# Performance work log

Hardware: AMD Instinct MI355X
Metric: run time of the kernel (lower is better)

Reference implementation:

```python
import jax, jax.numpy as jnp
import numpy as np

L, P, D, NH, RBF, NL = 256, 1024, 256, 4, 50, 2
HD = D // NH
EPS = 1e-5


def _layernorm(x, g, b):
    mu = x.mean(-1, keepdims=True)
    var = ((x - mu) ** 2).mean(-1, keepdims=True)
    return (x - mu) * jax.lax.rsqrt(var + EPS) * g + b


def setup_inputs() -> dict:
    key = jax.random.key(0)
    ks = iter(jax.random.split(key, 64))
    def nrm(shape, s=0.02):
        return jax.random.normal(next(ks), shape, dtype=jnp.float32) * s
    inp = {
        "protein_features": jax.random.normal(next(ks), (1, P, 20), jnp.float32),
        "ligand_features": jax.random.normal(next(ks), (1, L, 20), jnp.float32),
        "protein_positions": jax.random.normal(next(ks), (1, P, 3), jnp.float32),
        "ligand_positions": jax.random.normal(next(ks), (1, L, 3), jnp.float32),
        "pair_rbf": jax.random.uniform(next(ks), (1, L, P, RBF), jnp.float32),
        # encoders
        "pe_w1": nrm((20, D)), "pe_b1": jnp.zeros((D,)),
        "pe_w2": nrm((D, D)), "pe_b2": jnp.zeros((D,)),
        "le_w1": nrm((20, D)), "le_b1": jnp.zeros((D,)),
        "le_w2": nrm((D, D)), "le_b2": jnp.zeros((D,)),
        # cross-attn layers stacked over NL
        "qw": nrm((NL, D, D)), "qb": jnp.zeros((NL, D)),
        "kw": nrm((NL, D, D)), "kb": jnp.zeros((NL, D)),
        "vw": nrm((NL, D, D)), "vb": jnp.zeros((NL, D)),
        "rw": nrm((NL, RBF, NH)), "rb": jnp.zeros((NL, NH)),
        "ow": nrm((NL, D, D)), "ob": jnp.zeros((NL, D)),
        "ln_g": jnp.ones((NL, D)), "ln_b": jnp.zeros((NL, D)),
        # gated pooling
        "pg_w1": nrm((D, D // 2)), "pg_b1": jnp.zeros((D // 2,)),
        "pg_w2": nrm((D // 2, 1)), "pg_b2": jnp.zeros((1,)),
        # heads
        "af_w1": nrm((D, D)), "af_b1": jnp.zeros((D,)),
        "af_w2": nrm((D, 1)), "af_b2": jnp.zeros((1,)),
        "cf_w1": nrm((D, D // 2)), "cf_b1": jnp.zeros((D // 2,)),
        "cf_w2": nrm((D // 2, 1)), "cf_b2": jnp.zeros((1,)),
        "iw1": nrm((2 * D + RBF, D)), "ib1": jnp.zeros((D,)),
        "iw2": nrm((D, 5)), "ib2": jnp.zeros((5,)),
    }
    return inp


def reference(protein_features, ligand_features, protein_positions, ligand_positions,
              pair_rbf, pe_w1, pe_b1, pe_w2, pe_b2, le_w1, le_b1, le_w2, le_b2,
              qw, qb, kw, kb, vw, vb, rw, rb, ow, ob, ln_g, ln_b,
              pg_w1, pg_b1, pg_w2, pg_b2, af_w1, af_b1, af_w2, af_b2,
              cf_w1, cf_b1, cf_w2, cf_b2, iw1, ib1, iw2, ib2):
    pf = protein_features[0]          # [P, 20]
    lf = ligand_features[0]           # [L, 20]
    rbf = pair_rbf[0]                 # [L, P, RBF]

    prot_h = jax.nn.silu(pf @ pe_w1 + pe_b1) @ pe_w2 + pe_b2   # [P, D]
    lig_h = jax.nn.silu(lf @ le_w1 + le_b1) @ le_w2 + le_b2    # [L, D]

    scale = float(HD) ** 0.5
    attn_w = None
    for i in range(NL):
        Q = (lig_h @ qw[i] + qb[i]).reshape(L, NH, HD)
        K = (prot_h @ kw[i] + kb[i]).reshape(P, NH, HD)
        V = (prot_h @ vw[i] + vb[i]).reshape(P, NH, HD)
        scores = jnp.einsum('lhd,phd->lph', Q, K) / scale      # [L, P, NH]
        scores = scores + (rbf @ rw[i] + rb[i])                # RBF additive bias per head
        attn_w = jax.nn.softmax(scores, axis=1)                # softmax over protein axis
        attended = jnp.einsum('lph,phd->lhd', attn_w, V).reshape(L, D)
        lig_h = _layernorm(lig_h + attended @ ow[i] + ob[i], ln_g[i], ln_b[i])

    gate_logits = jnp.tanh(lig_h @ pg_w1 + pg_b1) @ pg_w2 + pg_b2  # [L, 1]
    gate = jax.nn.softmax(gate_logits, axis=0)
    complex_repr = (gate * lig_h).sum(axis=0, keepdims=True)        # [1, D]

    pkd = jax.nn.silu(complex_repr @ af_w1 + af_b1) @ af_w2 + af_b2
    conf = jax.nn.sigmoid(jax.nn.silu(complex_repr @ cf_w1 + cf_b1) @ cf_w2 + cf_b2)
    docking_score = pkd * conf

    lig_exp = jnp.broadcast_to(lig_h[:, None, :], (L, P, D))
    prot_exp = jnp.broadcast_to(prot_h[None, :, :], (L, P, D))
    pair_input = jnp.concatenate([lig_exp, prot_exp, rbf], axis=-1)  # [L, P, 2D+RBF]
    imap = jax.nn.sigmoid(jax.nn.silu(pair_input @ iw1 + ib1) @ iw2 + ib2)

    attn_out = attn_w.mean(axis=-1).reshape(1, L * P)
    return (docking_score, pkd, conf, imap[None], attn_out)
```

## Files before the change

### kernel.cpp

```cpp
#include <hip/hip_runtime.h>
#include <math.h>

#define LN_ 256
#define PN_ 1024
#define DN_ 256
#define NH_ 4
#define RBF_N 50
#define NL_ 2
#define HD_ 64
#define EPSV 1e-5f
#define LP_ (LN_ * PN_)

__device__ __forceinline__ float fast_sigmoid(float x){ return 1.f/(1.f+__expf(-x)); }
__device__ __forceinline__ float fast_silu(float x){ return x/(1.f+__expf(-x)); }

struct GSeg {
  const float* A; const float* W; const float* bias; float* C;
  int K; int act; int transOut;
};
struct GArgs { GSeg s[3]; int b0, b1; };

__global__ __launch_bounds__(256) void gemm8(GArgs ga)
{
  extern __shared__ float sA[];
  int bid = blockIdx.x;
  int si = (bid < ga.b0) ? 0 : (bid < ga.b1 ? 1 : 2);
  int base = (si == 0) ? 0 : ((si == 1) ? ga.b0 : ga.b1);
  GSeg sg = ga.s[si];
  int row0 = (bid - base) * 8;
  int K = sg.K;
  int t = threadIdx.x;
  for (int idx = t; idx < 8 * K; idx += 256) {
    int r = idx / K, k = idx - r * K;
    sA[idx] = sg.A[(size_t)(row0 + r) * K + k];
  }
  __syncthreads();
  float acc[8];
  float bv = sg.bias ? sg.bias[t] : 0.f;
  #pragma unroll
  for (int r = 0; r < 8; r++) acc[r] = bv;
  for (int k = 0; k < K; k++) {
    float w = sg.W[(size_t)k * DN_ + t];
    #pragma unroll
    for (int r = 0; r < 8; r++) acc[r] = fmaf(sA[r * K + k], w, acc[r]);
  }
  #pragma unroll
  for (int r = 0; r < 8; r++) {
    float v = acc[r];
    if (sg.act == 1) v = fast_silu(v);
    if (sg.transOut) sg.C[(size_t)t * PN_ + row0 + r] = v;
    else             sg.C[(size_t)(row0 + r) * DN_ + t] = v;
  }
}

__global__ __launch_bounds__(256) void rbf_transpose(
    const float* __restrict__ rbf, float* __restrict__ rbfT)
{
  __shared__ float ld[256][RBF_N + 1];
  int t = threadIdx.x;
  size_t base = (size_t)blockIdx.x << 8;
  const float* src = rbf + base * RBF_N;
  for (int i = 0; i < RBF_N; i++) {
    int fl = i * 256 + t;
    int row = fl / RBF_N, col = fl - row * RBF_N;
    ld[row][col] = src[fl];
  }
  __syncthreads();
  for (int k = 0; k < RBF_N; k++)
    rbfT[(size_t)k * LP_ + base + t] = ld[t][k];
}

__global__ __launch_bounds__(256) void scores_softmax_l(
    const float* __restrict__ Q, const float* __restrict__ Kt,
    const float* __restrict__ rbfT, const float* __restrict__ rw,
    const float* __restrict__ rb, float* __restrict__ attn,
    float* __restrict__ amean)
{
  int l = blockIdx.x, t = threadIdx.x, lane = t & 63, wv = t >> 6;
  __shared__ float qs[DN_];
  __shared__ float rws[NH_][RBF_N];
  __shared__ float redm[16], reds[16];
  qs[t] = Q[(size_t)l * DN_ + t];
  if (t < RBF_N * NH_) rws[t & 3][t >> 2] = rw[t];
  __syncthreads();

  float sc[NH_][4];
  for (int i = 0; i < 4; i++) {
    int p = t + (i << 8);
    size_t idx = ((size_t)l << 10) + p;
    float s2[NH_] = {0.f, 0.f, 0.f, 0.f};
    #pragma unroll 10
    for (int k = 0; k < RBF_N; k++) {
      float rv = rbfT[(size_t)k * LP_ + idx];
      s2[0] = fmaf(rv, rws[0][k], s2[0]);
      s2[1] = fmaf(rv, rws[1][k], s2[1]);
      s2[2] = fmaf(rv, rws[2][k], s2[2]);
      s2[3] = fmaf(rv, rws[3][k], s2[3]);
    }
    #pragma unroll
    for (int h = 0; h < NH_; h++) {
      const float* kp = Kt + ((size_t)(h << 6) << 10) + p;
      float a = 0.f;
      #pragma unroll 8
      for (int d = 0; d < HD_; d++) a = fmaf(qs[(h << 6) + d], kp[(size_t)d << 10], a);
      sc[h][i] = a * 0.125f + s2[h] + rb[h];
    }
  }

  float mh[NH_];
  #pragma unroll
  for (int h = 0; h < NH_; h++) {
    float m = fmaxf(fmaxf(sc[h][0], sc[h][1]), fmaxf(sc[h][2], sc[h][3]));
    for (int o = 32; o > 0; o >>= 1) m = fmaxf(m, __shfl_xor(m, o));
    if (lane == 0) redm[h * 4 + wv] = m;
  }
  __syncthreads();
  #pragma unroll
  for (int h = 0; h < NH_; h++)
    mh[h] = fmaxf(fmaxf(redm[h * 4 + 0], redm[h * 4 + 1]),
                  fmaxf(redm[h * 4 + 2], redm[h * 4 + 3]));

  float e[NH_][4], inv[NH_];
  #pragma unroll
  for (int h = 0; h < NH_; h++) {
    float s = 0.f;
    #pragma unroll
    for (int i = 0; i < 4; i++) { e[h][i] = __expf(sc[h][i] - mh[h]); s += e[h][i]; }
    for (int o = 32; o > 0; o >>= 1) s += __shfl_xor(s, o);
    if (lane == 0) reds[h * 4 + wv] = s;
  }
  __syncthreads();
  #pragma unroll
  for (int h = 0; h < NH_; h++)
    inv[h] = 1.f / (reds[h * 4 + 0] + reds[h * 4 + 1] + reds[h * 4 + 2] + reds[h * 4 + 3]);

  #pragma unroll
  for (int h = 0; h < NH_; h++)
    for (int i = 0; i < 4; i++)
      attn[(((size_t)(l << 2) + h) << 10) + t + (i << 8)] = e[h][i] * inv[h];

  if (amean) {
    for (int i = 0; i < 4; i++) {
      float s = e[0][i] * inv[0] + e[1][i] * inv[1] + e[2][i] * inv[2] + e[3][i] * inv[3];
      amean[((size_t)l << 10) + t + (i << 8)] = s * 0.25f;
    }
  }
}

__global__ __launch_bounds__(256) void attend_proj_ln(
    const float* __restrict__ attn, const float* __restrict__ V,
    const float* __restrict__ ow, const float* __restrict__ ob,
    const float* __restrict__ g, const float* __restrict__ bb,
    float* __restrict__ lig)
{
  int l = blockIdx.x, t = threadIdx.x, lane = t & 63, wv = t >> 6;
  int h = t >> 6, d = t & 63;
  __shared__ float as[DN_];
  __shared__ float red[8];
  const float* aw = attn + (((size_t)(l << 2) + h) << 10);
  const float* Vp = V + (h << 6) + d;
  float acc = 0.f;
  #pragma unroll 8
  for (int p = 0; p < PN_; p++) acc = fmaf(aw[p], Vp[(size_t)p << 8], acc);
  as[t] = acc;
  __syncthreads();
  float acc2 = ob[t];
  #pragma unroll 4
  for (int k = 0; k < DN_; k++) acc2 = fmaf(as[k], ow[(size_t)(k << 8) + t], acc2);
  float x = lig[((size_t)l << 8) + t] + acc2;
  float sm = x;
  for (int o = 32; o > 0; o >>= 1) sm += __shfl_xor(sm, o);
  if (lane == 0) red[wv] = sm;
  __syncthreads();
  float mu = (red[0] + red[1] + red[2] + red[3]) * (1.f / DN_);
  float dx = x - mu;
  float v = dx * dx;
  for (int o = 32; o > 0; o >>= 1) v += __shfl_xor(v, o);
  if (lane == 0) red[4 + wv] = v;
  __syncthreads();
  float var = (red[4] + red[5] + red[6] + red[7]) * (1.f / DN_);
  lig[((size_t)l << 8) + t] = dx * (1.f / sqrtf(var + EPSV)) * g[t] + bb[t];
}

__global__ __launch_bounds__(128) void gate_logits_k(
    const float* __restrict__ lig, const float* __restrict__ w1,
    const float* __restrict__ b1, const float* __restrict__ w2,
    const float* __restrict__ b2, float* __restrict__ glog)
{
  int l = blockIdx.x, n = threadIdx.x, lane = n & 63, wv = n >> 6;
  __shared__ float ls[DN_];
  __shared__ float red[2];
  ls[n] = lig[(size_t)l * DN_ + n];
  ls[n + 128] = lig[(size_t)l * DN_ + n + 128];
  __syncthreads();
  float acc = b1[n];
  #pragma unroll 4
  for (int k = 0; k < DN_; k++) acc = fmaf(ls[k], w1[k * 128 + n], acc);
  float part = tanhf(acc) * w2[n];
  for (int o = 32; o > 0; o >>= 1) part += __shfl_xor(part, o);
  if (lane == 0) red[wv] = part;
  __syncthreads();
  if (n == 0) glog[l] = red[0] + red[1] + b2[0];
}

__global__ __launch_bounds__(256) void pool_heads(
    const float* __restrict__ lig, const float* __restrict__ glog,
    const float* __restrict__ afw1, const float* __restrict__ afb1,
    const float* __restrict__ afw2, const float* __restrict__ afb2,
    const float* __restrict__ cfw1, const float* __restrict__ cfb1,
    const float* __restrict__ cfw2, const float* __restrict__ cfb2,
    float* __restrict__ out)
{
  __shared__ float wsh[LN_];
  __shared__ float cr[DN_];
  __shared__ float h1s[DN_];
  __shared__ float h2s[128];
  __shared__ float red[8];
  int t = threadIdx.x, lane = t & 63, wv = t >> 6;
  float x = glog[t];
  float m = x;
  for (int o = 32; o > 0; o >>= 1) m = fmaxf(m, __shfl_xor(m, o));
  if (lane == 0) red[wv] = m;
  __syncthreads();
  m = fmaxf(fmaxf(red[0], red[1]), fmaxf(red[2], red[3]));
  float e = __expf(x - m);
  float s = e;
  for (int o = 32; o > 0; o >>= 1) s += __shfl_xor(s, o);
  if (lane == 0) red[4 + wv] = s;
  __syncthreads();
  s = red[4] + red[5] + red[6] + red[7];
  wsh[t] = e / s;
  __syncthreads();
  float acc = 0.f;
  #pragma unroll 4
  for (int l2 = 0; l2 < LN_; l2++) acc = fmaf(wsh[l2], lig[(size_t)l2 * DN_ + t], acc);
  cr[t] = acc;
  __syncthreads();
  float a = afb1[t];
  #pragma unroll 4
  for (int d = 0; d < DN_; d++) a = fmaf(cr[d], afw1[d * DN_ + t], a);
  h1s[t] = fast_silu(a);
  if (t < 128) {
    float c = cfb1[t];
    #pragma unroll 4
    for (int d = 0; d < DN_; d++) c = fmaf(cr[d], cfw1[d * 128 + t], c);
    h2s[t] = fast_silu(c);
  }
  __syncthreads();
  float pp = h1s[t] * afw2[t];
  for (int o = 32; o > 0; o >>= 1) pp += __shfl_xor(pp, o);
  if (lane == 0) red[wv] = pp;
  float cp = (t < 128) ? h2s[t] * cfw2[t] : 0.f;
  for (int o = 32; o > 0; o >>= 1) cp += __shfl_xor(cp, o);
  if (lane == 0) red[4 + wv] = cp;
  __syncthreads();
  if (t == 0) {
    float pkd = red[0] + red[1] + red[2] + red[3] + afb2[0];
    float cl  = red[4] + red[5] + red[6] + red[7] + cfb2[0];
    float conf = fast_sigmoid(cl);
    out[0] = pkd * conf;
    out[1] = pkd;
    out[2] = conf;
  }
}

__global__ __launch_bounds__(256, 4) void pair_main2(
    const float* __restrict__ A, const float* __restrict__ BT,
    const float* __restrict__ rbfT, const float* __restrict__ Wr,
    const float* __restrict__ w2, const float* __restrict__ ib2,
    float* __restrict__ imap)
{
  int t = threadIdx.x;
  int bid = blockIdx.x;
  int l = bid >> 2;
  int p = ((bid & 3) << 8) + t;
  size_t idx = ((size_t)l << 10) + p;
  const float* Ar = A + (l << 8);
  float acc[5];
  #pragma unroll
  for (int o = 0; o < 5; o++) acc[o] = ib2[o];

  for (int dt = 0; dt < 4; dt++) {
    int d0 = dt << 6;
    float h[64];
    #pragma unroll
    for (int j = 0; j < 64; j++)
      h[j] = Ar[d0 + j] + BT[(size_t)(d0 + j) * PN_ + p];

    #pragma unroll 2
    for (int k = 0; k < RBF_N; k++) {
      float rv = rbfT[(size_t)k * LP_ + idx];
      const float* wr = Wr + k * DN_ + d0;
      #pragma unroll
      for (int j = 0; j < 64; j++)
        h[j] = fmaf(rv, wr[j], h[j]);
    }

    #pragma unroll
    for (int j = 0; j < 64; j++) {
      float sh = fast_silu(h[j]);
      const float* w2r = w2 + (size_t)(d0 + j) * 5;
      #pragma unroll
      for (int o = 0; o < 5; o++) acc[o] = fmaf(sh, w2r[o], acc[o]);
    }
  }
  float* op = imap + idx * 5;
  #pragma unroll
  for (int o = 0; o < 5; o++) op[o] = fast_sigmoid(acc[o]);
}

extern "C" void kernel_launch(void* const* d_in, const int* in_sizes, int n_in,
                              void* d_out, int out_size, void* d_ws, size_t ws_size,
                              hipStream_t stream)
{
  const float* pf    = (const float*)d_in[0];
  const float* lf    = (const float*)d_in[1];
  const float* rbf   = (const float*)d_in[4];
  const float* pe_w1 = (const float*)d_in[5];
  const float* pe_b1 = (const float*)d_in[6];
  const float* pe_w2 = (const float*)d_in[7];
  const float* pe_b2 = (const float*)d_in[8];
  const float* le_w1 = (const float*)d_in[9];
  const float* le_b1 = (const float*)d_in[10];
  const float* le_w2 = (const float*)d_in[11];
  const float* le_b2 = (const float*)d_in[12];
  const float* qw = (const float*)d_in[13];
  const float* qb = (const float*)d_in[14];
  const float* kw = (const float*)d_in[15];
  const float* kb = (const float*)d_in[16];
  const float* vw = (const float*)d_in[17];
  const float* vb = (const float*)d_in[18];
  const float* rw = (const float*)d_in[19];
  const float* rb = (const float*)d_in[20];
  const float* ow = (const float*)d_in[21];
  const float* ob = (const float*)d_in[22];
  const float* ln_g = (const float*)d_in[23];
  const float* ln_b = (const float*)d_in[24];
  const float* pg_w1 = (const float*)d_in[25];
  const float* pg_b1 = (const float*)d_in[26];
  const float* pg_w2 = (const float*)d_in[27];
  const float* pg_b2 = (const float*)d_in[28];
  const float* af_w1 = (const float*)d_in[29];
  const float* af_b1 = (const float*)d_in[30];
  const float* af_w2 = (const float*)d_in[31];
  const float* af_b2 = (const float*)d_in[32];
  const float* cf_w1 = (const float*)d_in[33];
  const float* cf_b1 = (const float*)d_in[34];
  const float* cf_w2 = (const float*)d_in[35];
  const float* cf_b2 = (const float*)d_in[36];
  const float* iw1 = (const float*)d_in[37];
  const float* ib1 = (const float*)d_in[38];
  const float* iw2 = (const float*)d_in[39];
  const float* ib2 = (const float*)d_in[40];

  float* out = (float*)d_out;

  float* w = (float*)d_ws;
  size_t off = 0;
  float* prot_h = w + off; off += (size_t)PN_ * DN_;
  float* lig_h  = w + off; off += (size_t)LN_ * DN_;
  float* ph1    = w + off; off += (size_t)PN_ * DN_;
  float* lh1    = w + off; off += (size_t)LN_ * DN_;
  float* Qb     = w + off; off += (size_t)LN_ * DN_;
  float* Kt     = w + off; off += (size_t)DN_ * PN_;
  float* Vb     = w + off; off += (size_t)PN_ * DN_;
  float* attn   = w + off; off += (size_t)LN_ * NH_ * PN_;
  float* pairA  = w + off; off += (size_t)LN_ * DN_;
  float* glog   = w + off; off += LN_;
  off = (off + 255) & ~(size_t)255;
  float* rbfT   = w + off; off += (size_t)RBF_N * LP_;

  const int PB = PN_ / 8;
  const int LB = LN_ / 8;
  const size_t smax = 8 * DN_ * sizeof(float);

  rbf_transpose<<<LP_ / 256, 256, 0, stream>>>(rbf, rbfT);

  {
    GArgs ga;
    ga.s[0] = { pf, pe_w1, pe_b1, ph1, 20, 1, 0 };
    ga.s[1] = { lf, le_w1, le_b1, lh1, 20, 1, 0 };
    ga.s[2] = ga.s[1];
    ga.b0 = PB; ga.b1 = PB + LB;
    gemm8<<<PB + LB, 256, smax, stream>>>(ga);
  }
  {
    GArgs ga;
    ga.s[0] = { ph1, pe_w2, pe_b2, prot_h, DN_, 0, 0 };
    ga.s[1] = { lh1, le_w2, le_b2, lig_h, DN_, 0, 0 };
    ga.s[2] = ga.s[1];
    ga.b0 = PB; ga.b1 = PB + LB;
    gemm8<<<PB + LB, 256, smax, stream>>>(ga);
  }

  for (int i = 0; i < NL_; i++) {
    const size_t wo = (size_t)i * DN_ * DN_;
    {
      GArgs ga;
      ga.s[0] = { lig_h,  qw + wo, qb + i * DN_, Qb, DN_, 0, 0 };
      ga.s[1] = { prot_h, kw + wo, kb + i * DN_, Kt, DN_, 0, 1 };
      ga.s[2] = { prot_h, vw + wo, vb + i * DN_, Vb, DN_, 0, 0 };
      ga.b0 = LB; ga.b1 = LB + PB;
      gemm8<<<LB + 2 * PB, 256, smax, stream>>>(ga);
    }
    scores_softmax_l<<<LN_, 256, 0, stream>>>(
        Qb, Kt, rbfT, rw + (size_t)i * RBF_N * NH_, rb + i * NH_, attn,
        (i == NL_ - 1) ? (out + 3 + (size_t)LN_ * PN_ * 5) : nullptr);
    attend_proj_ln<<<LN_, 256, 0, stream>>>(attn, Vb, ow + wo, ob + i * DN_,
                                            ln_g + i * DN_, ln_b + i * DN_, lig_h);
  }

  gate_logits_k<<<LN_, 128, 0, stream>>>(lig_h, pg_w1, pg_b1, pg_w2, pg_b2, glog);
  pool_heads<<<1, 256, 0, stream>>>(lig_h, glog, af_w1, af_b1, af_w2, af_b2,
                                    cf_w1, cf_b1, cf_w2, cf_b2, out);

  {
    GArgs ga;
    ga.s[0] = { lig_h,  iw1,                       ib1,     pairA, DN_, 0, 0 };
    ga.s[1] = { prot_h, iw1 + (size_t)DN_ * DN_,   nullptr, Kt,    DN_, 0, 1 };
    ga.s[2] = ga.s[1];
    ga.b0 = LB; ga.b1 = LB + PB;
    gemm8<<<LB + PB, 256, smax, stream>>>(ga);
  }

  pair_main2<<<LP_ / 256, 256, 0, stream>>>(
      pairA, Kt, rbfT, iw1 + (size_t)2 * DN_ * DN_, iw2, ib2, out + 3);
}
```

Before: 732.7 us.

## Use bf16 MFMA for pair-map RBF projection and widen blocks in attention kernels

Replaces the scalar pair interaction kernel with one that stages RBF rows in LDS as bf16 and computes the RBF-to-hidden projection with 16x16x32 bf16 MFMA instructions, adding a one-off kernel that packs the RBF weight slice into transposed bf16. Separately, gemm8 now splits K across two thread halves, and the scores/softmax and attend/projection/layernorm kernels use 1024-thread blocks with one position per thread or split reductions. The goal is to remove the FMA-bound pair kernel and raise parallelism in the small per-ligand kernels. Running the RBF projection in bf16 lowers accuracy of the interaction map.

```diff
diff --git a/kernel.cpp b/kernel.cpp
--- a/kernel.cpp
+++ b/kernel.cpp
@@ -11,8 +11,16 @@
 #define EPSV 1e-5f
 #define LP_ (LN_ * PN_)
 
+typedef __attribute__((ext_vector_type(8))) short bf16x8;
+typedef __attribute__((ext_vector_type(4))) float f32x4;
+
 __device__ __forceinline__ float fast_sigmoid(float x){ return 1.f/(1.f+__expf(-x)); }
 __device__ __forceinline__ float fast_silu(float x){ return x/(1.f+__expf(-x)); }
+__device__ __forceinline__ short f2bf(float x){
+  union { float f; unsigned u; } v; v.f = x;
+  unsigned r = v.u + 0x7FFF + ((v.u >> 16) & 1);
+  return (short)(r >> 16);
+}
 
 struct GSeg {
   const float* A; const float* W; const float* bias; float* C;
@@ -20,9 +28,10 @@
 };
 struct GArgs { GSeg s[3]; int b0, b1; };
 
-__global__ __launch_bounds__(256) void gemm8(GArgs ga)
+__global__ __launch_bounds__(512) void gemm8(GArgs ga)
 {
   extern __shared__ float sA[];
+  __shared__ float part_[2][8][256];
   int bid = blockIdx.x;
   int si = (bid < ga.b0) ? 0 : (bid < ga.b1 ? 1 : 2);
   int base = (si == 0) ? 0 : ((si == 1) ? ga.b0 : ga.b1);
@@ -30,26 +39,33 @@
   int row0 = (bid - base) * 8;
   int K = sg.K;
   int t = threadIdx.x;
-  for (int idx = t; idx < 8 * K; idx += 256) {
+  int col = t & 255, half = t >> 8;
+  for (int idx = t; idx < 8 * K; idx += 512) {
     int r = idx / K, k = idx - r * K;
     sA[idx] = sg.A[(size_t)(row0 + r) * K + k];
   }
   __syncthreads();
   float acc[8];
-  float bv = sg.bias ? sg.bias[t] : 0.f;
-  #pragma unroll
-  for (int r = 0; r < 8; r++) acc[r] = bv;
-  for (int k = 0; k < K; k++) {
-    float w = sg.W[(size_t)k * DN_ + t];
+  #pragma unroll
+  for (int r = 0; r < 8; r++) acc[r] = 0.f;
+  int K2 = K >> 1;
+  for (int k = half * K2; k < half * K2 + K2; k++) {
+    float w = sg.W[(size_t)k * DN_ + col];
     #pragma unroll
     for (int r = 0; r < 8; r++) acc[r] = fmaf(sA[r * K + k], w, acc[r]);
   }
   #pragma unroll
-  for (int r = 0; r < 8; r++) {
-    float v = acc[r];
-    if (sg.act == 1) v = fast_silu(v);
-    if (sg.transOut) sg.C[(size_t)t * PN_ + row0 + r] = v;
-    else             sg.C[(size_t)(row0 + r) * DN_ + t] = v;
+  for (int r = 0; r < 8; r++) part_[half][r][col] = acc[r];
+  __syncthreads();
+  if (half == 0) {
+    float bv = sg.bias ? sg.bias[col] : 0.f;
+    #pragma unroll
+    for (int r = 0; r < 8; r++) {
+      float v = part_[0][r][col] + part_[1][r][col] + bv;
+      if (sg.act == 1) v = fast_silu(v);
+      if (sg.transOut) sg.C[(size_t)col * PN_ + row0 + r] = v;
+      else             sg.C[(size_t)(row0 + r) * DN_ + col] = v;
+    }
   }
 }
 
@@ -62,15 +78,23 @@
   const float* src = rbf + base * RBF_N;
   for (int i = 0; i < RBF_N; i++) {
     int fl = i * 256 + t;
-    int row = fl / RBF_N, col = fl - row * RBF_N;
-    ld[row][col] = src[fl];
+    int row = fl / RBF_N, colk = fl - row * RBF_N;
+    ld[row][colk] = src[fl];
   }
   __syncthreads();
   for (int k = 0; k < RBF_N; k++)
     rbfT[(size_t)k * LP_ + base + t] = ld[t][k];
 }
 
-__global__ __launch_bounds__(256) void scores_softmax_l(
+__global__ __launch_bounds__(256) void wr_pack(
+    const float* __restrict__ Wr, short* __restrict__ WT)
+{
+  int d = threadIdx.x;
+  for (int k = 0; k < 64; k++)
+    WT[d * 64 + k] = (k < RBF_N) ? f2bf(Wr[k * DN_ + d]) : (short)0;
+}
+
+__global__ __launch_bounds__(1024) void scores_softmax_l(
     const float* __restrict__ Q, const float* __restrict__ Kt,
     const float* __restrict__ rbfT, const float* __restrict__ rw,
     const float* __restrict__ rb, float* __restrict__ attn,
@@ -79,107 +103,109 @@
   int l = blockIdx.x, t = threadIdx.x, lane = t & 63, wv = t >> 6;
   __shared__ float qs[DN_];
   __shared__ float rws[NH_][RBF_N];
-  __shared__ float redm[16], reds[16];
-  qs[t] = Q[(size_t)l * DN_ + t];
+  __shared__ float redm[NH_][16], reds[NH_][16];
+  if (t < DN_) qs[t] = Q[(size_t)l * DN_ + t];
   if (t < RBF_N * NH_) rws[t & 3][t >> 2] = rw[t];
   __syncthreads();
 
-  float sc[NH_][4];
-  for (int i = 0; i < 4; i++) {
-    int p = t + (i << 8);
-    size_t idx = ((size_t)l << 10) + p;
-    float s2[NH_] = {0.f, 0.f, 0.f, 0.f};
-    #pragma unroll 10
-    for (int k = 0; k < RBF_N; k++) {
-      float rv = rbfT[(size_t)k * LP_ + idx];
-      s2[0] = fmaf(rv, rws[0][k], s2[0]);
-      s2[1] = fmaf(rv, rws[1][k], s2[1]);
-      s2[2] = fmaf(rv, rws[2][k], s2[2]);
-      s2[3] = fmaf(rv, rws[3][k], s2[3]);
-    }
-    #pragma unroll
-    for (int h = 0; h < NH_; h++) {
-      const float* kp = Kt + ((size_t)(h << 6) << 10) + p;
-      float a = 0.f;
-      #pragma unroll 8
-      for (int d = 0; d < HD_; d++) a = fmaf(qs[(h << 6) + d], kp[(size_t)d << 10], a);
-      sc[h][i] = a * 0.125f + s2[h] + rb[h];
-    }
-  }
-
+  int p = t;
+  size_t idx = ((size_t)l << 10) + p;
+  float s2[NH_] = {0.f, 0.f, 0.f, 0.f};
+  #pragma unroll 10
+  for (int k = 0; k < RBF_N; k++) {
+    float rv = rbfT[(size_t)k * LP_ + idx];
+    s2[0] = fmaf(rv, rws[0][k], s2[0]);
+    s2[1] = fmaf(rv, rws[1][k], s2[1]);
+    s2[2] = fmaf(rv, rws[2][k], s2[2]);
+    s2[3] = fmaf(rv, rws[3][k], s2[3]);
+  }
+  float sc[NH_];
+  #pragma unroll
+  for (int h = 0; h < NH_; h++) {
+    const float* kp = Kt + ((size_t)(h << 6) << 10) + p;
+    float a = 0.f;
+    #pragma unroll 8
+    for (int d = 0; d < HD_; d++) a = fmaf(qs[(h << 6) + d], kp[(size_t)d << 10], a);
+    sc[h] = a * 0.125f + s2[h] + rb[h];
+  }
+
+  #pragma unroll
+  for (int h = 0; h < NH_; h++) {
+    float m = sc[h];
+    for (int o = 32; o > 0; o >>= 1) m = fmaxf(m, __shfl_xor(m, o));
+    if (lane == 0) redm[h][wv] = m;
+  }
+  __syncthreads();
   float mh[NH_];
   #pragma unroll
   for (int h = 0; h < NH_; h++) {
-    float m = fmaxf(fmaxf(sc[h][0], sc[h][1]), fmaxf(sc[h][2], sc[h][3]));
-    for (int o = 32; o > 0; o >>= 1) m = fmaxf(m, __shfl_xor(m, o));
-    if (lane == 0) redm[h * 4 + wv] = m;
-  }
-  __syncthreads();
-  #pragma unroll
-  for (int h = 0; h < NH_; h++)
-    mh[h] = fmaxf(fmaxf(redm[h * 4 + 0], redm[h * 4 + 1]),
-                  fmaxf(redm[h * 4 + 2], redm[h * 4 + 3]));
-
-  float e[NH_][4], inv[NH_];
+    float m = redm[h][0];
+    for (int i = 1; i < 16; i++) m = fmaxf(m, redm[h][i]);
+    mh[h] = m;
+  }
+  float e[NH_];
   #pragma unroll
   for (int h = 0; h < NH_; h++) {
-    float s = 0.f;
-    #pragma unroll
-    for (int i = 0; i < 4; i++) { e[h][i] = __expf(sc[h][i] - mh[h]); s += e[h][i]; }
+    e[h] = __expf(sc[h] - mh[h]);
+    float s = e[h];
     for (int o = 32; o > 0; o >>= 1) s += __shfl_xor(s, o);
-    if (lane == 0) reds[h * 4 + wv] = s;
-  }
-  __syncthreads();
-  #pragma unroll
-  for (int h = 0; h < NH_; h++)
-    inv[h] = 1.f / (reds[h * 4 + 0] + reds[h * 4 + 1] + reds[h * 4 + 2] + reds[h * 4 + 3]);
-
-  #pragma unroll
-  for (int h = 0; h < NH_; h++)
-    for (int i = 0; i < 4; i++)
-      attn[(((size_t)(l << 2) + h) << 10) + t + (i << 8)] = e[h][i] * inv[h];
-
-  if (amean) {
-    for (int i = 0; i < 4; i++) {
-      float s = e[0][i] * inv[0] + e[1][i] * inv[1] + e[2][i] * inv[2] + e[3][i] * inv[3];
-      amean[((size_t)l << 10) + t + (i << 8)] = s * 0.25f;
-    }
-  }
-}
-
-__global__ __launch_bounds__(256) void attend_proj_ln(
+    if (lane == 0) reds[h][wv] = s;
+  }
+  __syncthreads();
+  float am = 0.f;
+  #pragma unroll
+  for (int h = 0; h < NH_; h++) {
+    float s = reds[h][0];
+    for (int i = 1; i < 16; i++) s += reds[h][i];
+    float a = e[h] / s;
+    attn[(((size_t)(l << 2) + h) << 10) + p] = a;
+    am += a;
+  }
+  if (amean) amean[idx] = am * 0.25f;
+}
+
+__global__ __launch_bounds__(1024) void attend_proj_ln(
     const float* __restrict__ attn, const float* __restrict__ V,
     const float* __restrict__ ow, const float* __restrict__ ob,
     const float* __restrict__ g, const float* __restrict__ bb,
     float* __restrict__ lig)
 {
-  int l = blockIdx.x, t = threadIdx.x, lane = t & 63, wv = t >> 6;
-  int h = t >> 6, d = t & 63;
-  __shared__ float as[DN_];
+  int l = blockIdx.x, t = threadIdx.x;
+  int q = t >> 8, col = t & 255, h = (t >> 6) & 3;
+  __shared__ float part[4][256];
+  __shared__ float as_[256];
   __shared__ float red[8];
   const float* aw = attn + (((size_t)(l << 2) + h) << 10);
-  const float* Vp = V + (h << 6) + d;
   float acc = 0.f;
-  #pragma unroll 8
-  for (int p = 0; p < PN_; p++) acc = fmaf(aw[p], Vp[(size_t)p << 8], acc);
-  as[t] = acc;
-  __syncthreads();
-  float acc2 = ob[t];
-  #pragma unroll 4
-  for (int k = 0; k < DN_; k++) acc2 = fmaf(as[k], ow[(size_t)(k << 8) + t], acc2);
-  float x = lig[((size_t)l << 8) + t] + acc2;
+  for (int p = q * 256; p < q * 256 + 256; p++)
+    acc = fmaf(aw[p], V[((size_t)p << 8) + col], acc);
+  part[q][col] = acc;
+  __syncthreads();
+  if (t < 256) as_[t] = part[0][t] + part[1][t] + part[2][t] + part[3][t];
+  __syncthreads();
+  float acc2 = 0.f;
+  for (int k = q * 64; k < q * 64 + 64; k++)
+    acc2 = fmaf(as_[k], ow[(size_t)(k << 8) + col], acc2);
+  part[q][col] = acc2;
+  __syncthreads();
+  float x = 0.f;
+  if (t < 256)
+    x = lig[((size_t)l << 8) + t] + ob[t]
+      + part[0][t] + part[1][t] + part[2][t] + part[3][t];
   float sm = x;
   for (int o = 32; o > 0; o >>= 1) sm += __shfl_xor(sm, o);
-  if (lane == 0) red[wv] = sm;
+  if (t < 256 && (t & 63) == 0) red[t >> 6] = sm;
   __syncthreads();
   float mu = (red[0] + red[1] + red[2] + red[3]) * (1.f / DN_);
   float dx = x - mu;
   float v = dx * dx;
   for (int o = 32; o > 0; o >>= 1) v += __shfl_xor(v, o);
-  if (lane == 0) red[4 + wv] = v;
-  __syncthreads();
-  float var = (red[4] + red[5] + red[6] + red[7]) * (1.f / DN_);
-  lig[((size_t)l << 8) + t] = dx * (1.f / sqrtf(var + EPSV)) * g[t] + bb[t];
+  if (t < 256 && (t & 63) == 0) red[4 + (t >> 6)] = v;
+  __syncthreads();
+  if (t < 256) {
+    float var = (red[4] + red[5] + red[6] + red[7]) * (1.f / DN_);
+    lig[((size_t)l << 8) + t] = dx * (1.f / sqrtf(var + EPSV)) * g[t] + bb[t];
+  }
 }
 
 __global__ __launch_bounds__(128) void gate_logits_k(
@@ -264,49 +290,126 @@
   }
 }
 
-__global__ __launch_bounds__(256, 4) void pair_main2(
+#define RSTR 72
+#define BTP 261
+__global__ __launch_bounds__(512) void pair_main3(
     const float* __restrict__ A, const float* __restrict__ BT,
-    const float* __restrict__ rbfT, const float* __restrict__ Wr,
+    const float* __restrict__ rbf, const short* __restrict__ WT,
     const float* __restrict__ w2, const float* __restrict__ ib2,
     float* __restrict__ imap)
 {
+  __shared__ short R_lds[256 * RSTR];
+  __shared__ float sBT[16 * BTP];
+  __shared__ float sw2[DN_ * 5];
+  __shared__ float sAl[DN_];
+
   int t = threadIdx.x;
+  int lane = t & 63, wid = t >> 6;
   int bid = blockIdx.x;
   int l = bid >> 2;
-  int p = ((bid & 3) << 8) + t;
-  size_t idx = ((size_t)l << 10) + p;
-  const float* Ar = A + (l << 8);
-  float acc[5];
-  #pragma unroll
-  for (int o = 0; o < 5; o++) acc[o] = ib2[o];
-
-  for (int dt = 0; dt < 4; dt++) {
-    int d0 = dt << 6;
-    float h[64];
-    #pragma unroll
-    for (int j = 0; j < 64; j++)
-      h[j] = Ar[d0 + j] + BT[(size_t)(d0 + j) * PN_ + p];
-
-    #pragma unroll 2
-    for (int k = 0; k < RBF_N; k++) {
-      float rv = rbfT[(size_t)k * LP_ + idx];
-      const float* wr = Wr + k * DN_ + d0;
+  int p0 = (bid & 3) << 8;
+
+  {
+    unsigned* rz = (unsigned*)R_lds;
+    #pragma unroll
+    for (int i = 0; i < 18; i++) rz[t + i * 512] = 0u;
+  }
+  __syncthreads();
+  {
+    const float* src = rbf + ((size_t)(l << 10) + p0) * RBF_N;
+    #pragma unroll
+    for (int i = 0; i < 25; i++) {
+      int idx = t + i * 512;
+      int row = idx / RBF_N, k = idx - row * RBF_N;
+      R_lds[row * RSTR + k] = f2bf(src[idx]);
+    }
+  }
+  for (int i = t; i < DN_ * 5; i += 512) sw2[i] = w2[i];
+  if (t < DN_) sAl[t] = A[((size_t)l << 8) + t];
+  __syncthreads();
+
+  int m = lane & 15, gq = lane >> 4;
+  int pt0 = wid * 2, pt1 = wid * 2 + 1;
+  bf16x8 a00 = *(const bf16x8*)&R_lds[(pt0 * 16 + m) * RSTR + 0 * 32 + gq * 8];
+  bf16x8 a01 = *(const bf16x8*)&R_lds[(pt0 * 16 + m) * RSTR + 1 * 32 + gq * 8];
+  bf16x8 a10 = *(const bf16x8*)&R_lds[(pt1 * 16 + m) * RSTR + 0 * 32 + gq * 8];
+  bf16x8 a11 = *(const bf16x8*)&R_lds[(pt1 * 16 + m) * RSTR + 1 * 32 + gq * 8];
+
+  float acc5[2][4][5];
+  #pragma unroll
+  for (int i = 0; i < 2; i++)
+    #pragma unroll
+    for (int r = 0; r < 4; r++)
       #pragma unroll
-      for (int j = 0; j < 64; j++)
-        h[j] = fmaf(rv, wr[j], h[j]);
+      for (int o = 0; o < 5; o++) acc5[i][r][o] = 0.f;
+
+  for (int nt = 0; nt < 16; nt++) {
+    __syncthreads();
+    #pragma unroll
+    for (int i = 0; i < 8; i++) {
+      int idx = t + i * 512;
+      int row = idx >> 8, colp = idx & 255;
+      sBT[row * BTP + colp] = BT[(size_t)((nt * 16 + row) << 10) + p0 + colp];
     }
-
-    #pragma unroll
-    for (int j = 0; j < 64; j++) {
-      float sh = fast_silu(h[j]);
-      const float* w2r = w2 + (size_t)(d0 + j) * 5;
+    __syncthreads();
+
+    int n = nt * 16 + m;
+    bf16x8 b0 = *(const bf16x8*)&WT[n * 64 + 0 * 32 + gq * 8];
+    bf16x8 b1 = *(const bf16x8*)&WT[n * 64 + 1 * 32 + gq * 8];
+
+    float bA = sAl[n];
+    #pragma unroll
+    for (int pi = 0; pi < 2; pi++) {
+      f32x4 acc = {0.f, 0.f, 0.f, 0.f};
+      if (pi == 0) {
+        acc = __builtin_amdgcn_mfma_f32_16x16x32_bf16(a00, b0, acc, 0, 0, 0);
+        acc = __builtin_amdgcn_mfma_f32_16x16x32_bf16(a01, b1, acc, 0, 0, 0);
+      } else {
+        acc = __builtin_amdgcn_mfma_f32_16x16x32_bf16(a10, b0, acc, 0, 0, 0);
+        acc = __builtin_amdgcn_mfma_f32_16x16x32_bf16(a11, b1, acc, 0, 0, 0);
+      }
+      int ptb = (pi == 0 ? pt0 : pt1) * 16 + gq * 4;
       #pragma unroll
-      for (int o = 0; o < 5; o++) acc[o] = fmaf(sh, w2r[o], acc[o]);
+      for (int r = 0; r < 4; r++) {
+        float bB = sBT[m * BTP + ptb + r];
+        float h = acc[r] + bA + bB;
+        float sh = fast_silu(h);
+        #pragma unroll
+        for (int o = 0; o < 5; o++)
+          acc5[pi][r][o] = fmaf(sh, sw2[n * 5 + o], acc5[pi][r][o]);
+      }
     }
   }
-  float* op = imap + idx * 5;
-  #pragma unroll
-  for (int o = 0; o < 5; o++) op[o] = fast_sigmoid(acc[o]);
+
+  #pragma unroll
+  for (int i = 0; i < 2; i++)
+    #pragma unroll
+    for (int r = 0; r < 4; r++)
+      #pragma unroll
+      for (int o = 0; o < 5; o++) {
+        float v = acc5[i][r][o];
+        v += __shfl_xor(v, 1);
+        v += __shfl_xor(v, 2);
+        v += __shfl_xor(v, 4);
+        v += __shfl_xor(v, 8);
+        acc5[i][r][o] = v;
+      }
+
+  if (m < 5) {
+    float bo = ib2[m];
+    #pragma unroll
+    for (int pi = 0; pi < 2; pi++) {
+      int ptb = (pi == 0 ? pt0 : pt1) * 16 + gq * 4;
+      #pragma unroll
+      for (int r = 0; r < 4; r++) {
+        float v = 0.f;
+        #pragma unroll
+        for (int o = 0; o < 5; o++) if (m == o) v = acc5[pi][r][o];
+        int p = p0 + ptb + r;
+        imap[((size_t)(l << 10) + p) * 5 + m] = fast_sigmoid(v + bo);
+      }
+    }
+  }
 }
 
 extern "C" void kernel_launch(void* const* d_in, const int* in_sizes, int n_in,
@@ -368,6 +471,8 @@
   float* pairA  = w + off; off += (size_t)LN_ * DN_;
   float* glog   = w + off; off += LN_;
   off = (off + 255) & ~(size_t)255;
+  float* WrBF   = w + off; off += (size_t)DN_ * 64 / 2;
+  off = (off + 255) & ~(size_t)255;
   float* rbfT   = w + off; off += (size_t)RBF_N * LP_;
 
   const int PB = PN_ / 8;
@@ -375,6 +480,7 @@
   const size_t smax = 8 * DN_ * sizeof(float);
 
   rbf_transpose<<<LP_ / 256, 256, 0, stream>>>(rbf, rbfT);
+  wr_pack<<<1, 256, 0, stream>>>(iw1 + (size_t)2 * DN_ * DN_, (short*)WrBF);
 
   {
     GArgs ga;
@@ -382,7 +488,7 @@
     ga.s[1] = { lf, le_w1, le_b1, lh1, 20, 1, 0 };
     ga.s[2] = ga.s[1];
     ga.b0 = PB; ga.b1 = PB + LB;
-    gemm8<<<PB + LB, 256, smax, stream>>>(ga);
+    gemm8<<<PB + LB, 512, smax, stream>>>(ga);
   }
   {
     GArgs ga;
@@ -390,7 +496,7 @@
     ga.s[1] = { lh1, le_w2, le_b2, lig_h, DN_, 0, 0 };
     ga.s[2] = ga.s[1];
     ga.b0 = PB; ga.b1 = PB + LB;
-    gemm8<<<PB + LB, 256, smax, stream>>>(ga);
+    gemm8<<<PB + LB, 512, smax, stream>>>(ga);
   }
 
   for (int i = 0; i < NL_; i++) {
@@ -401,13 +507,13 @@
       ga.s[1] = { prot_h, kw + wo, kb + i * DN_, Kt, DN_, 0, 1 };
       ga.s[2] = { prot_h, vw + wo, vb + i * DN_, Vb, DN_, 0, 0 };
       ga.b0 = LB; ga.b1 = LB + PB;
-      gemm8<<<LB + 2 * PB, 256, smax, stream>>>(ga);
+      gemm8<<<LB + 2 * PB, 512, smax, stream>>>(ga);
     }
-    scores_softmax_l<<<LN_, 256, 0, stream>>>(
+    scores_softmax_l<<<LN_, 1024, 0, stream>>>(
         Qb, Kt, rbfT, rw + (size_t)i * RBF_N * NH_, rb + i * NH_, attn,
         (i == NL_ - 1) ? (out + 3 + (size_t)LN_ * PN_ * 5) : nullptr);
-    attend_proj_ln<<<LN_, 256, 0, stream>>>(attn, Vb, ow + wo, ob + i * DN_,
-                                            ln_g + i * DN_, ln_b + i * DN_, lig_h);
+    attend_proj_ln<<<LN_, 1024, 0, stream>>>(attn, Vb, ow + wo, ob + i * DN_,
+                                             ln_g + i * DN_, ln_b + i * DN_, lig_h);
   }
 
   gate_logits_k<<<LN_, 128, 0, stream>>>(lig_h, pg_w1, pg_b1, pg_w2, pg_b2, glog);
@@ -420,9 +526,9 @@
     ga.s[1] = { prot_h, iw1 + (size_t)DN_ * DN_,   nullptr, Kt,    DN_, 0, 1 };
     ga.s[2] = ga.s[1];
     ga.b0 = LB; ga.b1 = LB + PB;
-    gemm8<<<LB + PB, 256, smax, stream>>>(ga);
-  }
-
-  pair_main2<<<LP_ / 256, 256, 0, stream>>>(
-      pairA, Kt, rbfT, iw1 + (size_t)2 * DN_ * DN_, iw2, ib2, out + 3);
-}
+    gemm8<<<LB + PB, 512, smax, stream>>>(ga);
+  }
+
+  pair_main3<<<LP_ / 256, 512, 0, stream>>>(
+      pairA, Kt, rbf, (const short*)WrBF, iw2, ib2, out + 3);
+}
```

After: 859.9 us. 17.4% more time.
